# Kernel tuning notes

Hardware: AMD Instinct MI355X
Metric: run time of the kernel (lower is better)

## Reference

```python
import jax, jax.numpy as jnp
import numpy as np

B, S, D = 1, 4096, 1024
H, G = 16, 4
DK = D // H            # 64, per-head dim
HKV = H // G           # 4 KV heads
DKV = D // G           # 256, KV projection width
SCALE = 1.0 / np.sqrt(np.float32(DK))


def setup_inputs() -> dict:
    key = jax.random.key(0)
    ks = jax.random.split(key, 10)
    std = 0.02
    return {
        "x": jax.random.normal(ks[0], (B, S, D), jnp.float32),
        "mask": jax.random.bernoulli(ks[1], 0.1, (B, 1, S)),  # True = masked out
        "Wq": jax.random.normal(ks[2], (D, D), jnp.float32) * std,
        "bq": jnp.zeros((D,), jnp.float32),
        "Wk": jax.random.normal(ks[3], (D, DKV), jnp.float32) * std,
        "bk": jnp.zeros((DKV,), jnp.float32),
        "Wv": jax.random.normal(ks[4], (D, DKV), jnp.float32) * std,
        "bv": jnp.zeros((DKV,), jnp.float32),
        "Wo": jax.random.normal(ks[5], (D, D), jnp.float32) * std,
        "bo": jnp.zeros((D,), jnp.float32),
    }


def reference(x, mask, Wq, bq, Wk, bk, Wv, bv, Wo, bo):
    b, s, _ = x.shape
    # projections
    q = (x @ Wq + bq).reshape(b, s, H, DK).transpose(0, 2, 1, 3)      # [B,H,S,DK]
    k = (x @ Wk + bk).reshape(b, s, HKV, DK).transpose(0, 2, 1, 3)    # [B,HKV,S,DK]
    v = (x @ Wv + bv).reshape(b, s, HKV, DK).transpose(0, 2, 1, 3)    # [B,HKV,S,DK]
    # expand KV heads: head h = kv_head * G + g (matches torch expand+reshape)
    k = jnp.repeat(k, G, axis=1)                                       # [B,H,S,DK]
    v = jnp.repeat(v, G, axis=1)                                       # [B,H,S,DK]
    scores = jnp.einsum("bhsd,bhtd->bhst", q, k) * SCALE              # [B,H,S,S]
    neg_inf = jnp.finfo(scores.dtype).min
    scores = jnp.where(mask[:, None, :, :], neg_inf, scores)           # mask: [B,1,1,S]
    attn = jax.nn.softmax(scores, axis=-1)
    out = jnp.einsum("bhst,bhtd->bhsd", attn, v)                      # [B,H,S,DK]
    out = out.transpose(0, 2, 1, 3).reshape(b, s, D)
    return out @ Wo + bo
```

## Files before the change

### kernel.cpp

```cpp
#include <hip/hip_runtime.h>
#include <cstdint>
#include <cstddef>

#define S_LEN 4096
#define DMODEL 1024
#define NHEADS 16
#define HDK 64
#define DKV 256
#define NTOT 1536
#define QSCALE 0.18033688011112042f

typedef __bf16 bf16;
typedef __bf16 bf16x8 __attribute__((ext_vector_type(8)));
typedef float f32x4 __attribute__((ext_vector_type(4)));

typedef __attribute__((address_space(3))) void lds_void;
typedef const __attribute__((address_space(1))) void gbl_void;

__device__ __forceinline__ void gload16(const void* g, void* l) {
  __builtin_amdgcn_global_load_lds((gbl_void*)g, (lds_void*)l, 16, 0, 0);
}

__global__ __launch_bounds__(256) void f32_to_bf16(
    const float* __restrict__ in, bf16* __restrict__ out, int n) {
  int i = (blockIdx.x * blockDim.x + threadIdx.x) * 8;
  if (i < n) {
    float4 a = *(const float4*)(in + i);
    float4 b = *(const float4*)(in + i + 4);
    bf16 o[8] = {(bf16)a.x, (bf16)a.y, (bf16)a.z, (bf16)a.w,
                 (bf16)b.x, (bf16)b.y, (bf16)b.z, (bf16)b.w};
    *(uint4*)(out + i) = *(uint4*)o;
  }
}

__global__ __launch_bounds__(256) void transpose_all(
    const float* __restrict__ Wq, const float* __restrict__ Wk,
    const float* __restrict__ Wv, const float* __restrict__ Wo,
    bf16* __restrict__ Wqt, bf16* __restrict__ Wkt,
    bf16* __restrict__ Wvt, bf16* __restrict__ Wot) {
  const float* src;
  bf16* dst;
  int C;
  switch (blockIdx.z) {
    case 0: src = Wq; dst = Wqt; C = DMODEL; break;
    case 1: src = Wk; dst = Wkt; C = DKV; break;
    case 2: src = Wv; dst = Wvt; C = DKV; break;
    default: src = Wo; dst = Wot; C = DMODEL; break;
  }
  const int c0 = blockIdx.x * 32;
  if (c0 >= C) return;
  __shared__ float tile[32][33];
  const int tx = threadIdx.x & 31;
  const int ty = threadIdx.x >> 5;
  const int r0 = blockIdx.y * 32;
#pragma unroll
  for (int i = 0; i < 4; i++)
    tile[ty + i * 8][tx] = src[(size_t)(r0 + ty + i * 8) * C + c0 + tx];
  __syncthreads();
#pragma unroll
  for (int i = 0; i < 4; i++)
    dst[(size_t)(c0 + ty + i * 8) * DMODEL + r0 + tx] = (bf16)tile[tx][ty + i * 8];
}

__global__ void mask_prep(const int* __restrict__ mask, float* __restrict__ mkf,
                          bf16* __restrict__ mkb, int n) {
  int i = blockIdx.x * blockDim.x + threadIdx.x;
  if (i < n) {
    float keep = mask[i] ? 0.0f : 1.0f;
    mkf[i] = keep;
    mkb[i] = (bf16)keep;
  }
}

template <int QKV>
__global__ __launch_bounds__(256) void gemm_ld(
    const bf16* __restrict__ A, const bf16* __restrict__ Bt, int M, int N, int K,
    const float* __restrict__ bq, const float* __restrict__ bk,
    const float* __restrict__ bv, const float* __restrict__ mkf,
    bf16* __restrict__ Qb, bf16* __restrict__ Kb, bf16* __restrict__ Vtb,
    const float* __restrict__ bo, float* __restrict__ Co) {
  __shared__ bf16 As[128 * 32];
  __shared__ bf16 Bs[128 * 32];
  const int t = threadIdx.x;
  const int lane = t & 63;
  const int wave = t >> 6;
  const int m0 = blockIdx.y * 128;
  const int n0 = blockIdx.x * 128;
  const int wm = (wave >> 1) * 64;
  const int wn = (wave & 1) * 64;
  const int lr = lane & 15;
  const int quad = lane >> 4;

  const int sr = lane >> 2;
  const int sc = (((lane & 3) ^ ((lane >> 3) & 3))) * 8;
  const int fq = (quad ^ ((lr >> 1) & 3)) * 8;

  f32x4 acc[4][4] = {};

  for (int k0 = 0; k0 < K; k0 += 32) {
    __syncthreads();
#pragma unroll
    for (int j = 0; j < 2; j++) {
      const int rbase = wave * 32 + j * 16;
      gload16(A + (size_t)(m0 + rbase + sr) * K + k0 + sc, &As[rbase * 32]);
      gload16(Bt + (size_t)(n0 + rbase + sr) * K + k0 + sc, &Bs[rbase * 32]);
    }
    __syncthreads();
    bf16x8 af[4], bfr[4];
#pragma unroll
    for (int mt = 0; mt < 4; mt++)
      af[mt] = *(const bf16x8*)(&As[(wm + mt * 16 + lr) * 32 + fq]);
#pragma unroll
    for (int nt = 0; nt < 4; nt++)
      bfr[nt] = *(const bf16x8*)(&Bs[(wn + nt * 16 + lr) * 32 + fq]);
#pragma unroll
    for (int mt = 0; mt < 4; mt++)
#pragma unroll
      for (int nt = 0; nt < 4; nt++)
        acc[mt][nt] = __builtin_amdgcn_mfma_f32_16x16x32_bf16(af[mt], bfr[nt], acc[mt][nt], 0, 0, 0);
  }

#pragma unroll
  for (int nt = 0; nt < 4; nt++) {
    const int n = n0 + wn + nt * 16 + lr;
    if (QKV) {
      if (n < DMODEL) {
        const float b = bq[n];
#pragma unroll
        for (int mt = 0; mt < 4; mt++)
#pragma unroll
          for (int r = 0; r < 4; r++) {
            const int m = m0 + wm + mt * 16 + quad * 4 + r;
            Qb[(size_t)m * DMODEL + n] = (bf16)((acc[mt][nt][r] + b) * QSCALE);
          }
      } else if (n < DMODEL + DKV) {
        const float b = bk[n - DMODEL];
#pragma unroll
        for (int mt = 0; mt < 4; mt++)
#pragma unroll
          for (int r = 0; r < 4; r++) {
            const int m = m0 + wm + mt * 16 + quad * 4 + r;
            Kb[(size_t)m * DKV + (n - DMODEL)] = (bf16)(acc[mt][nt][r] + b);
          }
      } else {
        const float b = bv[n - DMODEL - DKV];
#pragma unroll
        for (int mt = 0; mt < 4; mt++)
#pragma unroll
          for (int r = 0; r < 4; r++) {
            const int m = m0 + wm + mt * 16 + quad * 4 + r;
            Vtb[(size_t)(n - DMODEL - DKV) * S_LEN + m] = (bf16)((acc[mt][nt][r] + b) * mkf[m]);
          }
      }
    } else {
      const float b = bo[n];
#pragma unroll
      for (int mt = 0; mt < 4; mt++)
#pragma unroll
        for (int r = 0; r < 4; r++) {
          const int m = m0 + wm + mt * 16 + quad * 4 + r;
          Co[(size_t)m * N + n] = acc[mt][nt][r] + b;
        }
    }
  }
}

__global__ __launch_bounds__(256) void flash_attn(
    const bf16* __restrict__ Q, const bf16* __restrict__ K,
    const bf16* __restrict__ Vt, const bf16* __restrict__ mkb,
    bf16* __restrict__ O) {
  const int h = blockIdx.y;
  const int kvh = h >> 2;
  const int q0 = blockIdx.x * 128;
  const int t = threadIdx.x;
  const int lane = t & 63;
  const int wave = t >> 6;
  const int lr = lane & 15;
  const int quad = lane >> 4;

  __shared__ bf16 Ks[128][72];
  __shared__ bf16 Vs[64][136];
  __shared__ bf16 Ps[4][32][36];
  __shared__ bf16 mks[128];

  bf16x8 aq[2][2];
#pragma unroll
  for (int qt = 0; qt < 2; qt++) {
    const int qrow = q0 + wave * 32 + qt * 16 + lr;
    aq[qt][0] = *(const bf16x8*)(Q + (size_t)qrow * DMODEL + h * HDK + quad * 8);
    aq[qt][1] = *(const bf16x8*)(Q + (size_t)qrow * DMODEL + h * HDK + 32 + quad * 8);
  }

  f32x4 o_acc[2][4] = {};
  f32x4 l_acc[2] = {};

  for (int kv0 = 0; kv0 < S_LEN; kv0 += 128) {
    __syncthreads();
#pragma unroll
    for (int i = 0; i < 4; i++) {
      int id = t + i * 256;
      int row = id >> 3;
      int ch = (id & 7) * 8;
      uint4 d = *(const uint4*)(K + (size_t)(kv0 + row) * DKV + kvh * HDK + ch);
      *(uint4*)(&Ks[row][ch]) = d;
    }
#pragma unroll
    for (int i = 0; i < 4; i++) {
      int id = t + i * 256;
      int row = id >> 4;
      int ch = (id & 15) * 8;
      uint4 d = *(const uint4*)(Vt + (size_t)(kvh * HDK + row) * S_LEN + kv0 + ch);
      *(uint4*)(&Vs[row][ch]) = d;
    }
    if (t < 16) *(uint4*)(&mks[t * 8]) = *(const uint4*)(mkb + kv0 + t * 8);
    __syncthreads();

#pragma unroll
    for (int kc = 0; kc < 4; kc++) {
      bf16x8 ak[2][2];
#pragma unroll
      for (int ntl = 0; ntl < 2; ntl++) {
        const int krow = kc * 32 + ntl * 16 + lr;
        ak[ntl][0] = *(const bf16x8*)(&Ks[krow][quad * 8]);
        ak[ntl][1] = *(const bf16x8*)(&Ks[krow][32 + quad * 8]);
      }
#pragma unroll
      for (int qt = 0; qt < 2; qt++) {
#pragma unroll
        for (int ntl = 0; ntl < 2; ntl++) {
          f32x4 s = {};
          s = __builtin_amdgcn_mfma_f32_16x16x32_bf16(ak[ntl][0], aq[qt][0], s, 0, 0, 0);
          s = __builtin_amdgcn_mfma_f32_16x16x32_bf16(ak[ntl][1], aq[qt][1], s, 0, 0, 0);
          bf16 p4[4];
#pragma unroll
          for (int r = 0; r < 4; r++) p4[r] = (bf16)__builtin_amdgcn_exp2f(s[r]);
          *(uint2*)(&Ps[wave][qt * 16 + lr][ntl * 16 + quad * 4]) = *(uint2*)p4;
        }
      }
      bf16x8 bvf[4];
#pragma unroll
      for (int ntv = 0; ntv < 4; ntv++)
        bvf[ntv] = *(const bf16x8*)(&Vs[ntv * 16 + lr][kc * 32 + quad * 8]);
      bf16x8 mkfv = *(const bf16x8*)(&mks[kc * 32 + quad * 8]);
#pragma unroll
      for (int qt = 0; qt < 2; qt++) {
        bf16x8 ap = *(const bf16x8*)(&Ps[wave][qt * 16 + lr][quad * 8]);
#pragma unroll
        for (int ntv = 0; ntv < 4; ntv++)
          o_acc[qt][ntv] = __builtin_amdgcn_mfma_f32_16x16x32_bf16(ap, bvf[ntv], o_acc[qt][ntv], 0, 0, 0);
        l_acc[qt] = __builtin_amdgcn_mfma_f32_16x16x32_bf16(ap, mkfv, l_acc[qt], 0, 0, 0);
      }
    }
  }

#pragma unroll
  for (int qt = 0; qt < 2; qt++) {
#pragma unroll
    for (int ntv = 0; ntv < 4; ntv++) {
#pragma unroll
      for (int r = 0; r < 4; r++) {
        const int row = q0 + wave * 32 + qt * 16 + quad * 4 + r;
        O[(size_t)row * DMODEL + h * HDK + ntv * 16 + lr] =
            (bf16)(o_acc[qt][ntv][r] / l_acc[qt][r]);
      }
    }
  }
}

extern "C" void kernel_launch(void* const* d_in, const int* in_sizes, int n_in,
                              void* d_out, int out_size, void* d_ws, size_t ws_size,
                              hipStream_t stream) {
  const float* x = (const float*)d_in[0];
  const int* mask = (const int*)d_in[1];
  const float* Wq = (const float*)d_in[2];
  const float* bq = (const float*)d_in[3];
  const float* Wk = (const float*)d_in[4];
  const float* bk = (const float*)d_in[5];
  const float* Wv = (const float*)d_in[6];
  const float* bv = (const float*)d_in[7];
  const float* Wo = (const float*)d_in[8];
  const float* bo = (const float*)d_in[9];
  float* out = (float*)d_out;

  char* w = (char*)d_ws;
  bf16* xb  = (bf16*)w; w += (size_t)S_LEN * DMODEL * 2;
  bf16* Wqt = (bf16*)w; w += (size_t)DMODEL * DMODEL * 2;
  bf16* Wkt = (bf16*)w; w += (size_t)DKV * DMODEL * 2;
  bf16* Wvt = (bf16*)w; w += (size_t)DKV * DMODEL * 2;
  bf16* Wot = (bf16*)w; w += (size_t)DMODEL * DMODEL * 2;
  bf16* Qb  = (bf16*)w; w += (size_t)S_LEN * DMODEL * 2;
  bf16* Kb  = (bf16*)w; w += (size_t)S_LEN * DKV * 2;
  bf16* Vtb = (bf16*)w; w += (size_t)DKV * S_LEN * 2;
  bf16* Ob  = (bf16*)w; w += (size_t)S_LEN * DMODEL * 2;
  float* mkf = (float*)w; w += (size_t)S_LEN * 4;
  bf16* mkb = (bf16*)w; w += (size_t)S_LEN * 2;

  f32_to_bf16<<<dim3(S_LEN * DMODEL / (256 * 8)), 256, 0, stream>>>(x, xb, S_LEN * DMODEL);
  transpose_all<<<dim3(DMODEL / 32, DMODEL / 32, 4), 256, 0, stream>>>(
      Wq, Wk, Wv, Wo, Wqt, Wkt, Wvt, Wot);
  mask_prep<<<dim3(S_LEN / 256), 256, 0, stream>>>(mask, mkf, mkb, S_LEN);

  gemm_ld<1><<<dim3(NTOT / 128, S_LEN / 128), 256, 0, stream>>>(
      xb, Wqt, S_LEN, NTOT, DMODEL, bq, bk, bv, mkf, Qb, Kb, Vtb, nullptr, nullptr);

  flash_attn<<<dim3(S_LEN / 128, NHEADS), 256, 0, stream>>>(Qb, Kb, Vtb, mkb, Ob);

  gemm_ld<0><<<dim3(DMODEL / 128, S_LEN / 128), 256, 0, stream>>>(
      Ob, Wot, S_LEN, DMODEL, DMODEL, nullptr, nullptr, nullptr, nullptr,
      nullptr, nullptr, nullptr, bo, out);
}
```

Baseline: 245.3 us.

## Double GEMM K-tile to 64 and split attention KV tile across wave pairs

The projection GEMM now stages 64-wide K slices with a new XOR swizzle, which halves the number of barrier pairs per output tile. The flash attention kernel now has each wave handle 64 query rows over half of each 128-key tile instead of 32 query rows over the full tile. The two partial accumulators for each query block are then merged through shared memory at the end. This raises register use (o_acc 4x4) and LDS use (about 73KB), which may lower occupancy.

Result: slower. 275.3 us (+12.2%).

```diff
diff --git a/kernel.cpp b/kernel.cpp
--- a/kernel.cpp
+++ b/kernel.cpp
@@ -79,8 +79,8 @@
     const float* __restrict__ bv, const float* __restrict__ mkf,
     bf16* __restrict__ Qb, bf16* __restrict__ Kb, bf16* __restrict__ Vtb,
     const float* __restrict__ bo, float* __restrict__ Co) {
-  __shared__ bf16 As[128 * 32];
-  __shared__ bf16 Bs[128 * 32];
+  __shared__ bf16 As[128 * 64];
+  __shared__ bf16 Bs[128 * 64];
   const int t = threadIdx.x;
   const int lane = t & 63;
   const int wave = t >> 6;
@@ -91,33 +91,36 @@
   const int lr = lane & 15;
   const int quad = lane >> 4;
 
-  const int sr = lane >> 2;
-  const int sc = (((lane & 3) ^ ((lane >> 3) & 3))) * 8;
-  const int fq = (quad ^ ((lr >> 1) & 3)) * 8;
+  const int sr = lane >> 3;
+  const int sc = ((lane & 7) ^ (lane >> 3)) * 8;
 
   f32x4 acc[4][4] = {};
 
-  for (int k0 = 0; k0 < K; k0 += 32) {
+  for (int k0 = 0; k0 < K; k0 += 64) {
     __syncthreads();
 #pragma unroll
-    for (int j = 0; j < 2; j++) {
-      const int rbase = wave * 32 + j * 16;
-      gload16(A + (size_t)(m0 + rbase + sr) * K + k0 + sc, &As[rbase * 32]);
-      gload16(Bt + (size_t)(n0 + rbase + sr) * K + k0 + sc, &Bs[rbase * 32]);
+    for (int j = 0; j < 4; j++) {
+      const int rbase = wave * 32 + j * 8;
+      gload16(A + (size_t)(m0 + rbase + sr) * K + k0 + sc, &As[rbase * 64]);
+      gload16(Bt + (size_t)(n0 + rbase + sr) * K + k0 + sc, &Bs[rbase * 64]);
     }
     __syncthreads();
-    bf16x8 af[4], bfr[4];
-#pragma unroll
-    for (int mt = 0; mt < 4; mt++)
-      af[mt] = *(const bf16x8*)(&As[(wm + mt * 16 + lr) * 32 + fq]);
-#pragma unroll
-    for (int nt = 0; nt < 4; nt++)
-      bfr[nt] = *(const bf16x8*)(&Bs[(wn + nt * 16 + lr) * 32 + fq]);
-#pragma unroll
-    for (int mt = 0; mt < 4; mt++)
+#pragma unroll
+    for (int kh2 = 0; kh2 < 2; kh2++) {
+      const int fo = ((kh2 * 4 + quad) ^ (lr & 7)) * 8;
+      bf16x8 af[4], bfr[4];
+#pragma unroll
+      for (int mt = 0; mt < 4; mt++)
+        af[mt] = *(const bf16x8*)(&As[(wm + mt * 16 + lr) * 64 + fo]);
 #pragma unroll
       for (int nt = 0; nt < 4; nt++)
-        acc[mt][nt] = __builtin_amdgcn_mfma_f32_16x16x32_bf16(af[mt], bfr[nt], acc[mt][nt], 0, 0, 0);
+        bfr[nt] = *(const bf16x8*)(&Bs[(wn + nt * 16 + lr) * 64 + fo]);
+#pragma unroll
+      for (int mt = 0; mt < 4; mt++)
+#pragma unroll
+        for (int nt = 0; nt < 4; nt++)
+          acc[mt][nt] = __builtin_amdgcn_mfma_f32_16x16x32_bf16(af[mt], bfr[nt], acc[mt][nt], 0, 0, 0);
+    }
   }
 
 #pragma unroll
@@ -175,24 +178,27 @@
   const int t = threadIdx.x;
   const int lane = t & 63;
   const int wave = t >> 6;
+  const int qh = wave >> 1;
+  const int kh = wave & 1;
   const int lr = lane & 15;
   const int quad = lane >> 4;
 
-  __shared__ bf16 Ks[128][72];
-  __shared__ bf16 Vs[64][136];
-  __shared__ bf16 Ps[4][32][36];
-  __shared__ bf16 mks[128];
-
-  bf16x8 aq[2][2];
-#pragma unroll
-  for (int qt = 0; qt < 2; qt++) {
-    const int qrow = q0 + wave * 32 + qt * 16 + lr;
+  __shared__ __align__(16) char smem[72960];
+  bf16* Ks = (bf16*)smem;
+  bf16* Vs = (bf16*)(smem + 18432);
+  bf16* Ps = (bf16*)(smem + 35840);
+  bf16* mks = (bf16*)(smem + 72704);
+
+  bf16x8 aq[4][2];
+#pragma unroll
+  for (int qt = 0; qt < 4; qt++) {
+    const int qrow = q0 + qh * 64 + qt * 16 + lr;
     aq[qt][0] = *(const bf16x8*)(Q + (size_t)qrow * DMODEL + h * HDK + quad * 8);
     aq[qt][1] = *(const bf16x8*)(Q + (size_t)qrow * DMODEL + h * HDK + 32 + quad * 8);
   }
 
-  f32x4 o_acc[2][4] = {};
-  f32x4 l_acc[2] = {};
+  f32x4 o_acc[4][4] = {};
+  f32x4 l_acc[4] = {};
 
   for (int kv0 = 0; kv0 < S_LEN; kv0 += 128) {
     __syncthreads();
@@ -202,7 +208,7 @@
       int row = id >> 3;
       int ch = (id & 7) * 8;
       uint4 d = *(const uint4*)(K + (size_t)(kv0 + row) * DKV + kvh * HDK + ch);
-      *(uint4*)(&Ks[row][ch]) = d;
+      *(uint4*)(&Ks[row * 72 + ch]) = d;
     }
 #pragma unroll
     for (int i = 0; i < 4; i++) {
@@ -210,41 +216,42 @@
       int row = id >> 4;
       int ch = (id & 15) * 8;
       uint4 d = *(const uint4*)(Vt + (size_t)(kvh * HDK + row) * S_LEN + kv0 + ch);
-      *(uint4*)(&Vs[row][ch]) = d;
+      *(uint4*)(&Vs[row * 136 + ch]) = d;
     }
     if (t < 16) *(uint4*)(&mks[t * 8]) = *(const uint4*)(mkb + kv0 + t * 8);
     __syncthreads();
 
-#pragma unroll
-    for (int kc = 0; kc < 4; kc++) {
-      bf16x8 ak[2][2];
-#pragma unroll
-      for (int ntl = 0; ntl < 2; ntl++) {
-        const int krow = kc * 32 + ntl * 16 + lr;
-        ak[ntl][0] = *(const bf16x8*)(&Ks[krow][quad * 8]);
-        ak[ntl][1] = *(const bf16x8*)(&Ks[krow][32 + quad * 8]);
+    bf16x8 ak[4][2];
+#pragma unroll
+    for (int ntl = 0; ntl < 4; ntl++) {
+      const int krow = kh * 64 + ntl * 16 + lr;
+      ak[ntl][0] = *(const bf16x8*)(&Ks[krow * 72 + quad * 8]);
+      ak[ntl][1] = *(const bf16x8*)(&Ks[krow * 72 + 32 + quad * 8]);
+    }
+#pragma unroll
+    for (int qt = 0; qt < 4; qt++) {
+#pragma unroll
+      for (int ntl = 0; ntl < 4; ntl++) {
+        f32x4 s = {};
+        s = __builtin_amdgcn_mfma_f32_16x16x32_bf16(ak[ntl][0], aq[qt][0], s, 0, 0, 0);
+        s = __builtin_amdgcn_mfma_f32_16x16x32_bf16(ak[ntl][1], aq[qt][1], s, 0, 0, 0);
+        bf16 p4[4];
+#pragma unroll
+        for (int r = 0; r < 4; r++) p4[r] = (bf16)__builtin_amdgcn_exp2f(s[r]);
+        *(uint2*)(&Ps[(wave * 64 + qt * 16 + lr) * 72 + ntl * 16 + quad * 4]) = *(uint2*)p4;
       }
-#pragma unroll
-      for (int qt = 0; qt < 2; qt++) {
-#pragma unroll
-        for (int ntl = 0; ntl < 2; ntl++) {
-          f32x4 s = {};
-          s = __builtin_amdgcn_mfma_f32_16x16x32_bf16(ak[ntl][0], aq[qt][0], s, 0, 0, 0);
-          s = __builtin_amdgcn_mfma_f32_16x16x32_bf16(ak[ntl][1], aq[qt][1], s, 0, 0, 0);
-          bf16 p4[4];
-#pragma unroll
-          for (int r = 0; r < 4; r++) p4[r] = (bf16)__builtin_amdgcn_exp2f(s[r]);
-          *(uint2*)(&Ps[wave][qt * 16 + lr][ntl * 16 + quad * 4]) = *(uint2*)p4;
-        }
-      }
+    }
+#pragma unroll
+    for (int kc = 0; kc < 2; kc++) {
+      const int kbase = kh * 64 + kc * 32;
       bf16x8 bvf[4];
 #pragma unroll
       for (int ntv = 0; ntv < 4; ntv++)
-        bvf[ntv] = *(const bf16x8*)(&Vs[ntv * 16 + lr][kc * 32 + quad * 8]);
-      bf16x8 mkfv = *(const bf16x8*)(&mks[kc * 32 + quad * 8]);
-#pragma unroll
-      for (int qt = 0; qt < 2; qt++) {
-        bf16x8 ap = *(const bf16x8*)(&Ps[wave][qt * 16 + lr][quad * 8]);
+        bvf[ntv] = *(const bf16x8*)(&Vs[(ntv * 16 + lr) * 136 + kbase + quad * 8]);
+      bf16x8 mkfv = *(const bf16x8*)(&mks[kbase + quad * 8]);
+#pragma unroll
+      for (int qt = 0; qt < 4; qt++) {
+        bf16x8 ap = *(const bf16x8*)(&Ps[(wave * 64 + qt * 16 + lr) * 72 + kc * 32 + quad * 8]);
 #pragma unroll
         for (int ntv = 0; ntv < 4; ntv++)
           o_acc[qt][ntv] = __builtin_amdgcn_mfma_f32_16x16x32_bf16(ap, bvf[ntv], o_acc[qt][ntv], 0, 0, 0);
@@ -253,15 +260,37 @@
     }
   }
 
-#pragma unroll
-  for (int qt = 0; qt < 2; qt++) {
-#pragma unroll
-    for (int ntv = 0; ntv < 4; ntv++) {
-#pragma unroll
-      for (int r = 0; r < 4; r++) {
-        const int row = q0 + wave * 32 + qt * 16 + quad * 4 + r;
-        O[(size_t)row * DMODEL + h * HDK + ntv * 16 + lr] =
-            (bf16)(o_acc[qt][ntv][r] / l_acc[qt][r]);
+  __syncthreads();
+  float* fs = (float*)smem;
+  if (kh == 1) {
+#pragma unroll
+    for (int qt = 0; qt < 4; qt++) {
+#pragma unroll
+      for (int ntv = 0; ntv < 4; ntv++)
+#pragma unroll
+        for (int r = 0; r < 4; r++)
+          fs[qh * 5120 + (qt * 16 + ntv * 4 + r) * 64 + lane] = o_acc[qt][ntv][r];
+#pragma unroll
+      for (int r = 0; r < 4; r++)
+        fs[qh * 5120 + (64 + qt * 4 + r) * 64 + lane] = l_acc[qt][r];
+    }
+  }
+  __syncthreads();
+  if (kh == 0) {
+#pragma unroll
+    for (int qt = 0; qt < 4; qt++) {
+      float lsum[4];
+#pragma unroll
+      for (int r = 0; r < 4; r++)
+        lsum[r] = l_acc[qt][r] + fs[qh * 5120 + (64 + qt * 4 + r) * 64 + lane];
+#pragma unroll
+      for (int ntv = 0; ntv < 4; ntv++) {
+#pragma unroll
+        for (int r = 0; r < 4; r++) {
+          const float o = o_acc[qt][ntv][r] + fs[qh * 5120 + (qt * 16 + ntv * 4 + r) * 64 + lane];
+          const int row = q0 + qh * 64 + qt * 16 + quad * 4 + r;
+          O[(size_t)row * DMODEL + h * HDK + ntv * 16 + lr] = (bf16)(o / lsum[r]);
+        }
       }
     }
   }
```

## Merge prep kernels into one launch and double GEMM K-tile to 64

Applied to the files above, without the earlier changes.

The bf16 cast of x, the weight transposes and the mask preparation now run as one kernel, using extra z-slices of the grid, instead of three launches. Separately, the GEMM K-step grows from 32 to 64 with a wider XOR swizzle, which halves the number of barrier pairs per K loop and doubles LDS use per block. The aim is to cut launch overhead and synchronisation cost, at the price of higher LDS pressure that could lower occupancy.

Result: faster. 233.6 us (-4.8%).

```diff
diff --git a/kernel.cpp b/kernel.cpp
--- a/kernel.cpp
+++ b/kernel.cpp
@@ -21,54 +21,55 @@
   __builtin_amdgcn_global_load_lds((gbl_void*)g, (lds_void*)l, 16, 0, 0);
 }
 
-__global__ __launch_bounds__(256) void f32_to_bf16(
-    const float* __restrict__ in, bf16* __restrict__ out, int n) {
-  int i = (blockIdx.x * blockDim.x + threadIdx.x) * 8;
-  if (i < n) {
-    float4 a = *(const float4*)(in + i);
-    float4 b = *(const float4*)(in + i + 4);
-    bf16 o[8] = {(bf16)a.x, (bf16)a.y, (bf16)a.z, (bf16)a.w,
-                 (bf16)b.x, (bf16)b.y, (bf16)b.z, (bf16)b.w};
-    *(uint4*)(out + i) = *(uint4*)o;
-  }
-}
-
-__global__ __launch_bounds__(256) void transpose_all(
+__global__ __launch_bounds__(256) void prep(
+    const float* __restrict__ x, const int* __restrict__ mask,
     const float* __restrict__ Wq, const float* __restrict__ Wk,
     const float* __restrict__ Wv, const float* __restrict__ Wo,
+    bf16* __restrict__ xb, float* __restrict__ mkf, bf16* __restrict__ mkb,
     bf16* __restrict__ Wqt, bf16* __restrict__ Wkt,
     bf16* __restrict__ Wvt, bf16* __restrict__ Wot) {
-  const float* src;
-  bf16* dst;
-  int C;
-  switch (blockIdx.z) {
-    case 0: src = Wq; dst = Wqt; C = DMODEL; break;
-    case 1: src = Wk; dst = Wkt; C = DKV; break;
-    case 2: src = Wv; dst = Wvt; C = DKV; break;
-    default: src = Wo; dst = Wot; C = DMODEL; break;
-  }
-  const int c0 = blockIdx.x * 32;
-  if (c0 >= C) return;
-  __shared__ float tile[32][33];
-  const int tx = threadIdx.x & 31;
-  const int ty = threadIdx.x >> 5;
-  const int r0 = blockIdx.y * 32;
-#pragma unroll
-  for (int i = 0; i < 4; i++)
-    tile[ty + i * 8][tx] = src[(size_t)(r0 + ty + i * 8) * C + c0 + tx];
-  __syncthreads();
-#pragma unroll
-  for (int i = 0; i < 4; i++)
-    dst[(size_t)(c0 + ty + i * 8) * DMODEL + r0 + tx] = (bf16)tile[tx][ty + i * 8];
-}
-
-__global__ void mask_prep(const int* __restrict__ mask, float* __restrict__ mkf,
-                          bf16* __restrict__ mkb, int n) {
-  int i = blockIdx.x * blockDim.x + threadIdx.x;
-  if (i < n) {
-    float keep = mask[i] ? 0.0f : 1.0f;
-    mkf[i] = keep;
-    mkb[i] = (bf16)keep;
+  const int z = blockIdx.z;
+  if (z < 4) {
+    const float* src;
+    bf16* dst;
+    int C;
+    switch (z) {
+      case 0: src = Wq; dst = Wqt; C = DMODEL; break;
+      case 1: src = Wk; dst = Wkt; C = DKV; break;
+      case 2: src = Wv; dst = Wvt; C = DKV; break;
+      default: src = Wo; dst = Wot; C = DMODEL; break;
+    }
+    const int c0 = blockIdx.x * 32;
+    if (c0 >= C) return;
+    __shared__ float tile[32][33];
+    const int tx = threadIdx.x & 31;
+    const int ty = threadIdx.x >> 5;
+    const int r0 = blockIdx.y * 32;
+#pragma unroll
+    for (int i = 0; i < 4; i++)
+      tile[ty + i * 8][tx] = src[(size_t)(r0 + ty + i * 8) * C + c0 + tx];
+    __syncthreads();
+#pragma unroll
+    for (int i = 0; i < 4; i++)
+      dst[(size_t)(c0 + ty + i * 8) * DMODEL + r0 + tx] = (bf16)tile[tx][ty + i * 8];
+  } else {
+    const int b = blockIdx.y * 32 + blockIdx.x;
+    const int half = z - 4;
+    const int i = ((half * 1024 + b) * 256 + (int)threadIdx.x) * 8;
+    float4 a = *(const float4*)(x + i);
+    float4 c = *(const float4*)(x + i + 4);
+    bf16 o[8] = {(bf16)a.x, (bf16)a.y, (bf16)a.z, (bf16)a.w,
+                 (bf16)c.x, (bf16)c.y, (bf16)c.z, (bf16)c.w};
+    *(uint4*)(xb + i) = *(uint4*)o;
+    if (half == 1 && b < 2) {
+      const int mi = (b * 256 + (int)threadIdx.x) * 8;
+#pragma unroll
+      for (int j = 0; j < 8; j++) {
+        float keep = mask[mi + j] ? 0.0f : 1.0f;
+        mkf[mi + j] = keep;
+        mkb[mi + j] = (bf16)keep;
+      }
+    }
   }
 }
 
@@ -79,8 +80,8 @@
     const float* __restrict__ bv, const float* __restrict__ mkf,
     bf16* __restrict__ Qb, bf16* __restrict__ Kb, bf16* __restrict__ Vtb,
     const float* __restrict__ bo, float* __restrict__ Co) {
-  __shared__ bf16 As[128 * 32];
-  __shared__ bf16 Bs[128 * 32];
+  __shared__ bf16 As[128 * 64];
+  __shared__ bf16 Bs[128 * 64];
   const int t = threadIdx.x;
   const int lane = t & 63;
   const int wave = t >> 6;
@@ -91,33 +92,36 @@
   const int lr = lane & 15;
   const int quad = lane >> 4;
 
-  const int sr = lane >> 2;
-  const int sc = (((lane & 3) ^ ((lane >> 3) & 3))) * 8;
-  const int fq = (quad ^ ((lr >> 1) & 3)) * 8;
+  const int sr = lane >> 3;
+  const int sc = ((lane & 7) ^ (lane >> 3)) * 8;
 
   f32x4 acc[4][4] = {};
 
-  for (int k0 = 0; k0 < K; k0 += 32) {
-    __syncthreads();
-#pragma unroll
-    for (int j = 0; j < 2; j++) {
-      const int rbase = wave * 32 + j * 16;
-      gload16(A + (size_t)(m0 + rbase + sr) * K + k0 + sc, &As[rbase * 32]);
-      gload16(Bt + (size_t)(n0 + rbase + sr) * K + k0 + sc, &Bs[rbase * 32]);
-    }
-    __syncthreads();
-    bf16x8 af[4], bfr[4];
-#pragma unroll
-    for (int mt = 0; mt < 4; mt++)
-      af[mt] = *(const bf16x8*)(&As[(wm + mt * 16 + lr) * 32 + fq]);
-#pragma unroll
-    for (int nt = 0; nt < 4; nt++)
-      bfr[nt] = *(const bf16x8*)(&Bs[(wn + nt * 16 + lr) * 32 + fq]);
-#pragma unroll
-    for (int mt = 0; mt < 4; mt++)
+  for (int k0 = 0; k0 < K; k0 += 64) {
+    __syncthreads();
+#pragma unroll
+    for (int j = 0; j < 4; j++) {
+      const int rbase = wave * 32 + j * 8;
+      gload16(A + (size_t)(m0 + rbase + sr) * K + k0 + sc, &As[rbase * 64]);
+      gload16(Bt + (size_t)(n0 + rbase + sr) * K + k0 + sc, &Bs[rbase * 64]);
+    }
+    __syncthreads();
+#pragma unroll
+    for (int kh2 = 0; kh2 < 2; kh2++) {
+      const int fo = ((kh2 * 4 + quad) ^ (lr & 7)) * 8;
+      bf16x8 af[4], bfr[4];
+#pragma unroll
+      for (int mt = 0; mt < 4; mt++)
+        af[mt] = *(const bf16x8*)(&As[(wm + mt * 16 + lr) * 64 + fo]);
 #pragma unroll
       for (int nt = 0; nt < 4; nt++)
-        acc[mt][nt] = __builtin_amdgcn_mfma_f32_16x16x32_bf16(af[mt], bfr[nt], acc[mt][nt], 0, 0, 0);
+        bfr[nt] = *(const bf16x8*)(&Bs[(wn + nt * 16 + lr) * 64 + fo]);
+#pragma unroll
+      for (int mt = 0; mt < 4; mt++)
+#pragma unroll
+        for (int nt = 0; nt < 4; nt++)
+          acc[mt][nt] = __builtin_amdgcn_mfma_f32_16x16x32_bf16(af[mt], bfr[nt], acc[mt][nt], 0, 0, 0);
+    }
   }
 
 #pragma unroll
@@ -295,10 +299,8 @@
   float* mkf = (float*)w; w += (size_t)S_LEN * 4;
   bf16* mkb = (bf16*)w; w += (size_t)S_LEN * 2;
 
-  f32_to_bf16<<<dim3(S_LEN * DMODEL / (256 * 8)), 256, 0, stream>>>(x, xb, S_LEN * DMODEL);
-  transpose_all<<<dim3(DMODEL / 32, DMODEL / 32, 4), 256, 0, stream>>>(
-      Wq, Wk, Wv, Wo, Wqt, Wkt, Wvt, Wot);
-  mask_prep<<<dim3(S_LEN / 256), 256, 0, stream>>>(mask, mkf, mkb, S_LEN);
+  prep<<<dim3(32, 32, 6), 256, 0, stream>>>(
+      x, mask, Wq, Wk, Wv, Wo, xb, mkf, mkb, Wqt, Wkt, Wvt, Wot);
 
   gemm_ld<1><<<dim3(NTOT / 128, S_LEN / 128), 256, 0, stream>>>(
       xb, Wqt, S_LEN, NTOT, DMODEL, bq, bk, bv, mkf, Qb, Kb, Vtb, nullptr, nullptr);
```
